# Performance work log

Hardware: AMD Instinct MI355X
Metric: run time of the kernel (lower is better)

The kernel has to match this reference:

```python
import jax, jax.numpy as jnp
import numpy as np


def setup_inputs() -> dict:
    key = jax.random.key(0)
    kq, kk, kv = jax.random.split(key, 3)
    B, S, D = 4, 4096, 64
    q = jax.random.normal(kq, (B, S, D), dtype=jnp.float32)
    k = jax.random.normal(kk, (B, S, D), dtype=jnp.float32)
    v = jax.random.normal(kv, (B, S, D), dtype=jnp.float32)
    return {"q": q, "k": k, "v": v}


def reference(q, k, v):
    # Faithful math of the original blocked loop:
    #   output_i += exp(Q_i @ K_j^T) @ V_j, summed over all column blocks j
    # which is exactly unnormalized exponential attention:
    #   out = exp(Q K^T) V  (no 1/sqrt(d) scaling, no softmax normalization,
    #   no max-subtraction -- matching the source module's math).
    scores = jnp.einsum("bqd,bkd->bqk", q, k)  # [B, Sq, Sk]
    return jnp.einsum("bqk,bkd->bqd", jnp.exp(scores), v)  # [B, Sq, D]
```

## Files before the change

kernel.cpp:

```cpp
#include <hip/hip_runtime.h>
#include <hip/hip_bf16.h>


typedef short    s16x4 __attribute__((ext_vector_type(4)));
typedef short    s16x8 __attribute__((ext_vector_type(8)));
typedef _Float16 h16x8 __attribute__((ext_vector_type(8)));
typedef float    fx4   __attribute__((ext_vector_type(4)));
typedef float    fx16  __attribute__((ext_vector_type(16)));

constexpr int S = 4096, D = 64, BQ = 64, BN = 64;
constexpr int KH = 4;
constexpr int NT = S / BN / KH;
constexpr int KS_SH  = 64 * 72;
constexpr int BUF_SH = 2 * KS_SH;

__device__ __forceinline__ unsigned short f2bf(float x) {
    unsigned u = __float_as_uint(x);
    u = (u + 0x7FFFu + ((u >> 16) & 1u)) >> 16;
    return (unsigned short)u;
}
__device__ __forceinline__ float bf2f(unsigned short h) {
    return __uint_as_float(((unsigned)h) << 16);
}
__device__ __forceinline__ unsigned short f2h(float x) {
    union { _Float16 h; unsigned short s; } u;
    u.h = (_Float16)x;
    return u.s;
}
__device__ __forceinline__ unsigned packbf(float lo, float hi) {
    unsigned a = __float_as_uint(lo) + 0x8000u;
    unsigned b = __float_as_uint(hi) + 0x8000u;
    return __builtin_amdgcn_perm(b, a, 0x07060302u);
}

__global__ __launch_bounds__(256, 4) void attn_fused2(
    const float* __restrict__ q, const float* __restrict__ k,
    const float* __restrict__ v, float* __restrict__ partial)
{
    __shared__ unsigned short smem[2 * BUF_SH];

    const int tid = threadIdx.x, lane = tid & 63, w = tid >> 6;
    const int h = lane >> 5, m5 = lane & 31;
    const int mt = w & 1, kkh = w >> 1;
    const int b = blockIdx.y, q0 = blockIdx.x * BQ, kh = blockIdx.z;

    const float* kbase = k + ((size_t)b * S + (size_t)kh * NT * BN) * D;
    const float* vbase = v + ((size_t)b * S + (size_t)kh * NT * BN) * D;

    h16x8 qf[4];
    {
        const float* qrow = q + ((size_t)b * S + q0 + mt * 32 + m5) * D + h * 8;
        #pragma unroll
        for (int ks = 0; ks < 4; ++ks) {
            float4 a = *(const float4*)(qrow + ks * 16);
            float4 c = *(const float4*)(qrow + ks * 16 + 4);
            qf[ks] = (h16x8){(_Float16)a.x, (_Float16)a.y, (_Float16)a.z, (_Float16)a.w,
                             (_Float16)c.x, (_Float16)c.y, (_Float16)c.z, (_Float16)c.w};
        }
    }

    const int krow0 = tid >> 4;
    const int kc4   = (tid & 15) << 2;
    const int vd    = tid & 63;
    const int vg    = w;

    float4 kraw[4];
    float  vraw[16];

    auto load_raw = [&](int t) {
        const float* kt = kbase + (size_t)t * BN * D;
        const float* vt = vbase + (size_t)t * BN * D;
        #pragma unroll
        for (int i = 0; i < 4; ++i)
            kraw[i] = *(const float4*)(kt + (i * 16 + krow0) * D + kc4);
        #pragma unroll
        for (int j = 0; j < 16; ++j)
            vraw[j] = vt[(vg * 16 + j) * D + vd];
    };

    auto cvt_store = [&](int bi) {
        unsigned short* Ksb = smem + bi * BUF_SH;
        unsigned short* Vtb = Ksb + KS_SH;
        #pragma unroll
        for (int i = 0; i < 4; ++i) {
            s16x4 o = {(short)f2h(kraw[i].x), (short)f2h(kraw[i].y),
                       (short)f2h(kraw[i].z), (short)f2h(kraw[i].w)};
            *(s16x4*)&Ksb[(i * 16 + krow0) * 72 + kc4] = o;
        }
        union { unsigned u[4]; s16x8 v; } p0, p1;
        #pragma unroll
        for (int jj = 0; jj < 4; ++jj) {
            p0.u[jj] = packbf(vraw[2 * jj],     vraw[2 * jj + 1]);
            p1.u[jj] = packbf(vraw[8 + 2 * jj], vraw[9 + 2 * jj]);
        }
        *(s16x8*)&Vtb[vd * 72 + vg * 16]     = p0.v;
        *(s16x8*)&Vtb[vd * 72 + vg * 16 + 8] = p1.v;
    };

    fx16 oacc[2] = {};

    auto compute = [&](int bi) {
        const unsigned short* Ksb = smem + bi * BUF_SH;
        const unsigned short* Vtb = Ksb + KS_SH;

        fx16 sa = {};
        #pragma unroll
        for (int ks = 0; ks < 4; ++ks) {
            h16x8 a = *(const h16x8*)&Ksb[(kkh * 32 + m5) * 72 + ks * 16 + h * 8];
            sa = __builtin_amdgcn_mfma_f32_32x32x16_f16(a, qf[ks], sa, 0, 0, 0);
        }

        unsigned p01[8];
        #pragma unroll
        for (int rp = 0; rp < 8; ++rp)
            p01[rp] = packbf(__expf(sa[2 * rp]), __expf(sa[2 * rp + 1]));

        union frag { unsigned u[4]; s16x8 v; };
        frag A[2];
#if __has_builtin(__builtin_amdgcn_permlane32_swap)
        typedef unsigned uix2 __attribute__((ext_vector_type(2)));
        uix2 r0 = __builtin_amdgcn_permlane32_swap(p01[0], p01[2], false, false);
        uix2 r1 = __builtin_amdgcn_permlane32_swap(p01[1], p01[3], false, false);
        A[0].u[0] = r0.x; A[0].u[1] = r1.x; A[0].u[2] = r0.y; A[0].u[3] = r1.y;
        uix2 r2 = __builtin_amdgcn_permlane32_swap(p01[4], p01[6], false, false);
        uix2 r3 = __builtin_amdgcn_permlane32_swap(p01[5], p01[7], false, false);
        A[1].u[0] = r2.x; A[1].u[1] = r3.x; A[1].u[2] = r2.y; A[1].u[3] = r3.y;
#else
        unsigned sw[8];
        #pragma unroll
        for (int rp = 0; rp < 8; ++rp)
            sw[rp] = (unsigned)__shfl_xor((int)p01[rp], 32, 64);
        A[0].u[0] = h ? sw[2]  : p01[0];
        A[0].u[1] = h ? sw[3]  : p01[1];
        A[0].u[2] = h ? p01[2] : sw[0];
        A[0].u[3] = h ? p01[3] : sw[1];
        A[1].u[0] = h ? sw[6]  : p01[4];
        A[1].u[1] = h ? sw[7]  : p01[5];
        A[1].u[2] = h ? p01[6] : sw[4];
        A[1].u[3] = h ? p01[7] : sw[5];
#endif

        #pragma unroll
        for (int ss = 0; ss < 2; ++ss)
            #pragma unroll
            for (int dt = 0; dt < 2; ++dt) {
                s16x8 vv = *(const s16x8*)&Vtb[(dt * 32 + m5) * 72
                                               + kkh * 32 + ss * 16 + h * 8];
                oacc[dt] = __builtin_amdgcn_mfma_f32_32x32x16_bf16(
                    A[ss].v, vv, oacc[dt], 0, 0, 0);
            }
    };

    load_raw(0);
    cvt_store(0);
    load_raw(1);
    for (int t = 0; t < NT; ++t) {
        __syncthreads();
        if (t + 1 < NT) cvt_store((t + 1) & 1);
        if (t + 2 < NT) load_raw(t + 2);
        compute(t & 1);
    }

    __syncthreads();
    float* red = (float*)smem;
    if (kkh == 1) {
        #pragma unroll
        for (int dt = 0; dt < 2; ++dt)
            #pragma unroll
            for (int r = 0; r < 16; ++r)
                red[((mt * 2 + dt) * 16 + r) * 64 + lane] = oacc[dt][r];
    }
    __syncthreads();
    if (kkh == 0) {
        float* pout = partial + ((size_t)kh * 4 + b) * S * D;
        #pragma unroll
        for (int dt = 0; dt < 2; ++dt)
            #pragma unroll
            for (int r = 0; r < 16; ++r) {
                float val = oacc[dt][r] + red[((mt * 2 + dt) * 16 + r) * 64 + lane];
                int row = q0 + mt * 32 + (r & 3) + 8 * (r >> 2) + 4 * h;
                pout[(size_t)row * D + dt * 32 + m5] = val;
            }
    }
}

__global__ __launch_bounds__(256) void reduce4(
    const float4* __restrict__ p, float4* __restrict__ o, int n4, int stride4)
{
    int i = blockIdx.x * 256 + threadIdx.x;
    if (i < n4) {
        float4 a = p[i], b = p[i + stride4],
               c = p[i + 2 * stride4], d = p[i + 3 * stride4];
        o[i] = make_float4(a.x + b.x + c.x + d.x, a.y + b.y + c.y + d.y,
                           a.z + b.z + c.z + d.z, a.w + b.w + c.w + d.w);
    }
}

__global__ __launch_bounds__(1024) void attn_fallback(
    const float* __restrict__ q, const float* __restrict__ k,
    const float* __restrict__ v, float* __restrict__ out)
{
    __shared__ unsigned short Kh[64][72];
    __shared__ unsigned short Kl[64][72];
    __shared__ unsigned short Vs[64][68];
    __shared__ unsigned short Pf[64][72];

    const int tid = threadIdx.x, lane = tid & 63, wave = tid >> 6;
    const int quad = lane >> 4, tq = lane & 15;
    const int kkb = wave & 3, mba = wave >> 2;
    const int b = blockIdx.y, q0 = blockIdx.x * 64;
    const float* qb = q + (size_t)b * S * D;
    const float* kb = k + (size_t)b * S * D;
    const float* vb = v + (size_t)b * S * D;
    float* ob = out + (size_t)b * S * D;

    s16x8 qh[2], ql[2];
    {
        const float* qrow = qb + (size_t)(q0 + mba * 16 + tq) * D;
        #pragma unroll
        for (int ks = 0; ks < 2; ++ks) {
            const float* src = qrow + ks * 32 + quad * 8;
            float4 f0 = *(const float4*)src;
            float4 f1 = *(const float4*)(src + 4);
            float f[8] = {f0.x, f0.y, f0.z, f0.w, f1.x, f1.y, f1.z, f1.w};
            #pragma unroll
            for (int j = 0; j < 8; ++j) {
                unsigned short hh = f2bf(f[j]);
                qh[ks][j] = (short)hh;
                ql[ks][j] = (short)f2bf(f[j] - bf2f(hh));
            }
        }
    }
    fx4 oacc = {0.f, 0.f, 0.f, 0.f};
    const int krow = tid >> 4, kc4 = (tid & 15) << 2;
    const int vd = tid & 63, vk = (tid >> 6) << 2;

    for (int t = 0; t < S / 64; ++t) {
        __syncthreads();
        const float* kt = kb + (size_t)(t * 64 + krow) * D;
        const float* vt = vb + (size_t)(t * 64 + vk) * D;
        {
            float4 kv = *(const float4*)(kt + kc4);
            unsigned short h0 = f2bf(kv.x), h1 = f2bf(kv.y), h2 = f2bf(kv.z), h3 = f2bf(kv.w);
            s16x4 a = {(short)h0, (short)h1, (short)h2, (short)h3};
            s16x4 l4 = {(short)f2bf(kv.x - bf2f(h0)), (short)f2bf(kv.y - bf2f(h1)),
                        (short)f2bf(kv.z - bf2f(h2)), (short)f2bf(kv.w - bf2f(h3))};
            *(s16x4*)&Kh[krow][kc4] = a;
            *(s16x4*)&Kl[krow][kc4] = l4;
            const float* vs = vt + vd;
            s16x4 vv = {(short)f2bf(vs[0]), (short)f2bf(vs[D]),
                        (short)f2bf(vs[2 * D]), (short)f2bf(vs[3 * D])};
            *(s16x4*)&Vs[vd][vk] = vv;
        }
        __syncthreads();
        fx4 sacc = {0.f, 0.f, 0.f, 0.f};
        #pragma unroll
        for (int ks = 0; ks < 2; ++ks) {
            s16x8 kah = *(const s16x8*)&Kh[kkb * 16 + tq][ks * 32 + quad * 8];
            s16x8 kal = *(const s16x8*)&Kl[kkb * 16 + tq][ks * 32 + quad * 8];
            sacc = __builtin_amdgcn_mfma_f32_16x16x32_bf16(kah, qh[ks], sacc, 0, 0, 0);
            sacc = __builtin_amdgcn_mfma_f32_16x16x32_bf16(kah, ql[ks], sacc, 0, 0, 0);
            sacc = __builtin_amdgcn_mfma_f32_16x16x32_bf16(kal, qh[ks], sacc, 0, 0, 0);
        }
        s16x4 pp = {(short)f2bf(__expf(sacc[0])), (short)f2bf(__expf(sacc[1])),
                    (short)f2bf(__expf(sacc[2])), (short)f2bf(__expf(sacc[3]))};
        *(s16x4*)&Pf[mba * 16 + tq][kkb * 16 + (quad << 2)] = pp;
        __syncthreads();
        #pragma unroll
        for (int ks = 0; ks < 2; ++ks) {
            s16x8 pa = *(const s16x8*)&Pf[mba * 16 + tq][ks * 32 + quad * 8];
            const unsigned short* vr = &Vs[kkb * 16 + tq][ks * 32 + quad * 8];
            s16x4 va = *(const s16x4*)vr;
            s16x4 vb2 = *(const s16x4*)(vr + 4);
            s16x8 vfull = __builtin_shufflevector(va, vb2, 0, 1, 2, 3, 4, 5, 6, 7);
            oacc = __builtin_amdgcn_mfma_f32_16x16x32_bf16(pa, vfull, oacc, 0, 0, 0);
        }
    }
    #pragma unroll
    for (int r = 0; r < 4; ++r)
        ob[(size_t)(q0 + mba * 16 + quad * 4 + r) * D + kkb * 16 + tq] = oacc[r];
}

extern "C" void kernel_launch(void* const* d_in, const int* in_sizes, int n_in,
                              void* d_out, int out_size, void* d_ws, size_t ws_size,
                              hipStream_t stream) {
    const float* q = (const float*)d_in[0];
    const float* k = (const float*)d_in[1];
    const float* v = (const float*)d_in[2];
    float* out = (float*)d_out;
    const int nbatch = in_sizes[0] / (S * D);
    const size_t elems = (size_t)nbatch * S * D;

    const size_t need = (size_t)KH * elems * 4;
    if (nbatch == 4 && ws_size >= need && d_ws != nullptr) {
        float* partial = (float*)d_ws;
        dim3 grid(S / BQ, nbatch, KH);
        attn_fused2<<<grid, 256, 0, stream>>>(q, k, v, partial);
        const int n4 = (int)(elems / 4);
        reduce4<<<(n4 + 255) / 256, 256, 0, stream>>>(
            (const float4*)partial, (float4*)out, n4, n4);
    } else {
        dim3 grid(S / 64, nbatch);
        attn_fallback<<<grid, 1024, 0, stream>>>(q, k, v, out);
    }
}
```

Measured before the change: 100.2 us.

## Split keys eight ways, single-buffer LDS, raise occupancy, reorder grid for K/V locality

Doubles the key-split factor from 4 to 8, so each block handles half as many key tiles and the grid has twice as many blocks. It replaces the double-buffered LDS with a single buffer and two barriers per tile, and raises the occupancy hint to 8 waves per SIMD. The grid is reordered so batch and key-split vary fastest, which should help consecutive blocks share K/V tiles in cache. The cost is twice the partial-sum workspace traffic and an 8-way reduction, plus less overlap between loads and compute within a block.

```diff
diff --git a/kernel.cpp b/kernel.cpp
--- a/kernel.cpp
+++ b/kernel.cpp
@@ -9,10 +9,9 @@
 typedef float    fx16  __attribute__((ext_vector_type(16)));
 
 constexpr int S = 4096, D = 64, BQ = 64, BN = 64;
-constexpr int KH = 4;
+constexpr int KH = 8;
 constexpr int NT = S / BN / KH;
-constexpr int KS_SH  = 64 * 72;
-constexpr int BUF_SH = 2 * KS_SH;
+constexpr int KS_SH = 64 * 72;
 
 __device__ __forceinline__ unsigned short f2bf(float x) {
     unsigned u = __float_as_uint(x);
@@ -33,16 +32,17 @@
     return __builtin_amdgcn_perm(b, a, 0x07060302u);
 }
 
-__global__ __launch_bounds__(256, 4) void attn_fused2(
+__global__ __launch_bounds__(256, 8) void attn_fused3(
     const float* __restrict__ q, const float* __restrict__ k,
     const float* __restrict__ v, float* __restrict__ partial)
 {
-    __shared__ unsigned short smem[2 * BUF_SH];
+    __shared__ unsigned short smem[2 * KS_SH];
 
     const int tid = threadIdx.x, lane = tid & 63, w = tid >> 6;
     const int h = lane >> 5, m5 = lane & 31;
     const int mt = w & 1, kkh = w >> 1;
-    const int b = blockIdx.y, q0 = blockIdx.x * BQ, kh = blockIdx.z;
+    const int b = blockIdx.x & 3, kh = blockIdx.x >> 2;
+    const int q0 = blockIdx.y * BQ;
 
     const float* kbase = k + ((size_t)b * S + (size_t)kh * NT * BN) * D;
     const float* vbase = v + ((size_t)b * S + (size_t)kh * NT * BN) * D;
@@ -78,9 +78,9 @@
             vraw[j] = vt[(vg * 16 + j) * D + vd];
     };
 
-    auto cvt_store = [&](int bi) {
-        unsigned short* Ksb = smem + bi * BUF_SH;
-        unsigned short* Vtb = Ksb + KS_SH;
+    auto cvt_store = [&]() {
+        unsigned short* Ksb = smem;
+        unsigned short* Vtb = smem + KS_SH;
         #pragma unroll
         for (int i = 0; i < 4; ++i) {
             s16x4 o = {(short)f2h(kraw[i].x), (short)f2h(kraw[i].y),
@@ -99,9 +99,9 @@
 
     fx16 oacc[2] = {};
 
-    auto compute = [&](int bi) {
-        const unsigned short* Ksb = smem + bi * BUF_SH;
-        const unsigned short* Vtb = Ksb + KS_SH;
+    auto compute = [&]() {
+        const unsigned short* Ksb = smem;
+        const unsigned short* Vtb = smem + KS_SH;
 
         fx16 sa = {};
         #pragma unroll
@@ -152,16 +152,14 @@
     };
 
     load_raw(0);
-    cvt_store(0);
-    load_raw(1);
     for (int t = 0; t < NT; ++t) {
-        __syncthreads();
-        if (t + 1 < NT) cvt_store((t + 1) & 1);
-        if (t + 2 < NT) load_raw(t + 2);
-        compute(t & 1);
-    }
-
-    __syncthreads();
+        cvt_store();
+        __syncthreads();
+        if (t + 1 < NT) load_raw(t + 1);
+        compute();
+        __syncthreads();
+    }
+
     float* red = (float*)smem;
     if (kkh == 1) {
         #pragma unroll
@@ -184,15 +182,18 @@
     }
 }
 
-__global__ __launch_bounds__(256) void reduce4(
+__global__ __launch_bounds__(256) void reduce8(
     const float4* __restrict__ p, float4* __restrict__ o, int n4, int stride4)
 {
     int i = blockIdx.x * 256 + threadIdx.x;
     if (i < n4) {
-        float4 a = p[i], b = p[i + stride4],
-               c = p[i + 2 * stride4], d = p[i + 3 * stride4];
-        o[i] = make_float4(a.x + b.x + c.x + d.x, a.y + b.y + c.y + d.y,
-                           a.z + b.z + c.z + d.z, a.w + b.w + c.w + d.w);
+        float4 acc = p[i];
+        #pragma unroll
+        for (int j = 1; j < KH; ++j) {
+            float4 x = p[i + (size_t)j * stride4];
+            acc.x += x.x; acc.y += x.y; acc.z += x.z; acc.w += x.w;
+        }
+        o[i] = acc;
     }
 }
 
@@ -294,10 +295,10 @@
     const size_t need = (size_t)KH * elems * 4;
     if (nbatch == 4 && ws_size >= need && d_ws != nullptr) {
         float* partial = (float*)d_ws;
-        dim3 grid(S / BQ, nbatch, KH);
-        attn_fused2<<<grid, 256, 0, stream>>>(q, k, v, partial);
+        dim3 grid(nbatch * KH, S / BQ);
+        attn_fused3<<<grid, 256, 0, stream>>>(q, k, v, partial);
         const int n4 = (int)(elems / 4);
-        reduce4<<<(n4 + 255) / 256, 256, 0, stream>>>(
+        reduce8<<<(n4 + 255) / 256, 256, 0, stream>>>(
             (const float4*)partial, (float4*)out, n4, n4);
     } else {
         dim3 grid(S / 64, nbatch);
```

Result: slower. 226.3 us (+125.8%).

## Pre-convert K/V into MFMA fragment layout and stream via global_load_lds triple buffer

Applied to the files above, without the earlier changes.

Adds a prep kernel that converts K to fp16 and V to bf16 once per call, rearranging both into MFMA-fragment-ordered tiles in workspace. The attention kernel then streams these tiles straight into LDS with global_load_lds into a three-stage ring buffer, using waitcnt plus barrier. This removes the repeated per-block fp32 loads, conversion and transposed V stores, and halves the bytes read in the main loop. In exchange it adds a kernel launch, a workspace round trip, and a wraparound prefetch that issues redundant loads on the last iterations.

```diff
diff --git a/kernel.cpp b/kernel.cpp
--- a/kernel.cpp
+++ b/kernel.cpp
@@ -11,8 +11,9 @@
 constexpr int S = 4096, D = 64, BQ = 64, BN = 64;
 constexpr int KH = 4;
 constexpr int NT = S / BN / KH;
-constexpr int KS_SH  = 64 * 72;
-constexpr int BUF_SH = 2 * KS_SH;
+constexpr int NTILES = S / BN;
+constexpr int TILE_SH  = 8 * 512;
+constexpr int BATCH_SH = NTILES * TILE_SH;
 
 __device__ __forceinline__ unsigned short f2bf(float x) {
     unsigned u = __float_as_uint(x);
@@ -33,19 +34,65 @@
     return __builtin_amdgcn_perm(b, a, 0x07060302u);
 }
 
-__global__ __launch_bounds__(256, 4) void attn_fused2(
-    const float* __restrict__ q, const float* __restrict__ k,
-    const float* __restrict__ v, float* __restrict__ partial)
+__global__ __launch_bounds__(256) void prep3(
+    const float* __restrict__ k, const float* __restrict__ v,
+    unsigned short* __restrict__ kf, unsigned short* __restrict__ vf)
 {
-    __shared__ unsigned short smem[2 * BUF_SH];
+    __shared__ unsigned short tile[64 * 72];
+    const int tid   = threadIdx.x;
+    const int which = blockIdx.x & 1;
+    const int t     = (blockIdx.x >> 1) & 63;
+    const int b     = blockIdx.x >> 7;
+    const float* src = (which ? v : k) + ((size_t)b * S + t * BN) * D;
+
+    #pragma unroll
+    for (int i = 0; i < 4; ++i) {
+        int f   = i * 256 + tid;
+        int row = f >> 4;
+        int c4  = (f & 15) << 2;
+        float4 x = *(const float4*)(src + row * D + c4);
+        s16x4 o;
+        if (which) o = (s16x4){(short)f2bf(x.x), (short)f2bf(x.y),
+                               (short)f2bf(x.z), (short)f2bf(x.w)};
+        else       o = (s16x4){(short)f2h(x.x), (short)f2h(x.y),
+                               (short)f2h(x.z), (short)f2h(x.w)};
+        *(s16x4*)&tile[row * 72 + c4] = o;
+    }
+    __syncthreads();
+
+    const int l = tid & 63;
+    unsigned short* dst = (which ? vf : kf) + (size_t)b * BATCH_SH + t * TILE_SH;
+    #pragma unroll
+    for (int i = 0; i < 2; ++i) {
+        int c = (tid >> 6) * 2 + i;
+        s16x8 o;
+        if (which == 0) {
+            int row = (c >> 2) * 32 + (l & 31);
+            int col = (c & 3) * 16 + (l >> 5) * 8;
+            o = *(const s16x8*)&tile[row * 72 + col];
+        } else {
+            int r0  = (c >> 2) * 32 + ((c >> 1) & 1) * 16 + (l >> 5) * 8;
+            int col = (c & 1) * 32 + (l & 31);
+            #pragma unroll
+            for (int j = 0; j < 8; ++j) o[j] = (short)tile[(r0 + j) * 72 + col];
+        }
+        *(s16x8*)(dst + c * 512 + l * 8) = o;
+    }
+}
+
+__global__ __launch_bounds__(256, 4) void attn_s3(
+    const float* __restrict__ q, const unsigned short* __restrict__ kf,
+    const unsigned short* __restrict__ vf, float* __restrict__ partial)
+{
+    __shared__ unsigned short smem[3 * 2 * TILE_SH];
 
     const int tid = threadIdx.x, lane = tid & 63, w = tid >> 6;
     const int h = lane >> 5, m5 = lane & 31;
     const int mt = w & 1, kkh = w >> 1;
     const int b = blockIdx.y, q0 = blockIdx.x * BQ, kh = blockIdx.z;
 
-    const float* kbase = k + ((size_t)b * S + (size_t)kh * NT * BN) * D;
-    const float* vbase = v + ((size_t)b * S + (size_t)kh * NT * BN) * D;
+    const unsigned short* kfb = kf + (size_t)b * BATCH_SH + (size_t)kh * NT * TILE_SH;
+    const unsigned short* vfb = vf + (size_t)b * BATCH_SH + (size_t)kh * NT * TILE_SH;
 
     h16x8 qf[4];
     {
@@ -59,54 +106,45 @@
         }
     }
 
-    const int krow0 = tid >> 4;
-    const int kc4   = (tid & 15) << 2;
-    const int vd    = tid & 63;
-    const int vg    = w;
-
-    float4 kraw[4];
-    float  vraw[16];
-
-    auto load_raw = [&](int t) {
-        const float* kt = kbase + (size_t)t * BN * D;
-        const float* vt = vbase + (size_t)t * BN * D;
-        #pragma unroll
-        for (int i = 0; i < 4; ++i)
-            kraw[i] = *(const float4*)(kt + (i * 16 + krow0) * D + kc4);
-        #pragma unroll
-        for (int j = 0; j < 16; ++j)
-            vraw[j] = vt[(vg * 16 + j) * D + vd];
+    fx16 oacc[2] = {};
+
+    auto issue = [&](int t, int bi) {
+        unsigned short* base = &smem[bi * 2 * TILE_SH];
+        const size_t goff = (size_t)t * TILE_SH;
+        #pragma unroll
+        for (int i = 0; i < 2; ++i) {
+            const int c = w * 2 + i;
+            __builtin_amdgcn_global_load_lds(
+                (const __attribute__((address_space(1))) unsigned int*)
+                    (kfb + goff + c * 512 + lane * 8),
+                (__attribute__((address_space(3))) unsigned int*)
+                    (base + c * 512 + lane * 8), 16, 0, 0);
+            __builtin_amdgcn_global_load_lds(
+                (const __attribute__((address_space(1))) unsigned int*)
+                    (vfb + goff + c * 512 + lane * 8),
+                (__attribute__((address_space(3))) unsigned int*)
+                    (base + TILE_SH + c * 512 + lane * 8), 16, 0, 0);
+        }
     };
 
-    auto cvt_store = [&](int bi) {
-        unsigned short* Ksb = smem + bi * BUF_SH;
-        unsigned short* Vtb = Ksb + KS_SH;
-        #pragma unroll
-        for (int i = 0; i < 4; ++i) {
-            s16x4 o = {(short)f2h(kraw[i].x), (short)f2h(kraw[i].y),
-                       (short)f2h(kraw[i].z), (short)f2h(kraw[i].w)};
-            *(s16x4*)&Ksb[(i * 16 + krow0) * 72 + kc4] = o;
-        }
-        union { unsigned u[4]; s16x8 v; } p0, p1;
-        #pragma unroll
-        for (int jj = 0; jj < 4; ++jj) {
-            p0.u[jj] = packbf(vraw[2 * jj],     vraw[2 * jj + 1]);
-            p1.u[jj] = packbf(vraw[8 + 2 * jj], vraw[9 + 2 * jj]);
-        }
-        *(s16x8*)&Vtb[vd * 72 + vg * 16]     = p0.v;
-        *(s16x8*)&Vtb[vd * 72 + vg * 16 + 8] = p1.v;
-    };
-
-    fx16 oacc[2] = {};
-
-    auto compute = [&](int bi) {
-        const unsigned short* Ksb = smem + bi * BUF_SH;
-        const unsigned short* Vtb = Ksb + KS_SH;
+    issue(0, 0);
+    issue(1, 1);
+
+    for (int t = 0; t < NT; ++t) {
+        const int bi = t % 3;
+        __asm__ volatile("" ::: "memory");
+        __builtin_amdgcn_s_waitcnt(0x0F74);
+        __builtin_amdgcn_s_barrier();
+        __asm__ volatile("" ::: "memory");
+        issue((t + 2) & (NT - 1), (t + 2) % 3);
+
+        const unsigned short* Kb = &smem[bi * 2 * TILE_SH];
+        const unsigned short* Vb = Kb + TILE_SH;
 
         fx16 sa = {};
         #pragma unroll
         for (int ks = 0; ks < 4; ++ks) {
-            h16x8 a = *(const h16x8*)&Ksb[(kkh * 32 + m5) * 72 + ks * 16 + h * 8];
+            h16x8 a = *(const h16x8*)(Kb + (kkh * 4 + ks) * 512 + lane * 8);
             sa = __builtin_amdgcn_mfma_f32_32x32x16_f16(a, qf[ks], sa, 0, 0, 0);
         }
 
@@ -144,21 +182,11 @@
         for (int ss = 0; ss < 2; ++ss)
             #pragma unroll
             for (int dt = 0; dt < 2; ++dt) {
-                s16x8 vv = *(const s16x8*)&Vtb[(dt * 32 + m5) * 72
-                                               + kkh * 32 + ss * 16 + h * 8];
+                s16x8 vv = *(const s16x8*)(Vb + (kkh * 4 + ss * 2 + dt) * 512
+                                           + lane * 8);
                 oacc[dt] = __builtin_amdgcn_mfma_f32_32x32x16_bf16(
                     A[ss].v, vv, oacc[dt], 0, 0, 0);
             }
-    };
-
-    load_raw(0);
-    cvt_store(0);
-    load_raw(1);
-    for (int t = 0; t < NT; ++t) {
-        __syncthreads();
-        if (t + 1 < NT) cvt_store((t + 1) & 1);
-        if (t + 2 < NT) load_raw(t + 2);
-        compute(t & 1);
     }
 
     __syncthreads();
@@ -291,11 +319,15 @@
     const int nbatch = in_sizes[0] / (S * D);
     const size_t elems = (size_t)nbatch * S * D;
 
-    const size_t need = (size_t)KH * elems * 4;
+    const size_t need = elems * 2 * 2 + (size_t)KH * elems * 4;
     if (nbatch == 4 && ws_size >= need && d_ws != nullptr) {
-        float* partial = (float*)d_ws;
+        unsigned short* kf = (unsigned short*)d_ws;
+        unsigned short* vf = kf + elems;
+        float* partial = (float*)(vf + elems);
+
+        prep3<<<2 * nbatch * NTILES, 256, 0, stream>>>(k, v, kf, vf);
         dim3 grid(S / BQ, nbatch, KH);
-        attn_fused2<<<grid, 256, 0, stream>>>(q, k, v, partial);
+        attn_s3<<<grid, 256, 0, stream>>>(q, kf, vf, partial);
         const int n4 = (int)(elems / 4);
         reduce4<<<(n4 + 255) / 256, 256, 0, stream>>>(
             (const float4*)partial, (float4*)out, n4, n4);
```

New measurement: 96.70 us. -3.5%, faster.
